# Performance work log

Hardware: AMD Instinct MI355X
Metric: run time of the kernel (lower is better)

The kernel has to match this reference:

```python
import jax, jax.numpy as jnp
import numpy as np

HEAD_DIM = 64
N_HEADS = 16
D_S = N_HEADS * HEAD_DIM  # 1024
D_Z = 128


def setup_inputs() -> dict:
    key = jax.random.key(0)
    ks = jax.random.split(key, 12)
    B, S = 1, 1024
    sc = 0.02
    return {
        "s": jax.random.normal(ks[0], (B, S, D_S), jnp.float32),
        "z": jax.random.normal(ks[1], (B, S, S, D_Z), jnp.float32),
        "wq": jax.random.normal(ks[2], (N_HEADS * HEAD_DIM, D_S), jnp.float32) * sc,
        "bq": jax.random.normal(ks[3], (N_HEADS * HEAD_DIM,), jnp.float32) * sc,
        "wk": jax.random.normal(ks[4], (N_HEADS * HEAD_DIM, D_S), jnp.float32) * sc,
        "wv": jax.random.normal(ks[5], (N_HEADS * HEAD_DIM, D_S), jnp.float32) * sc,
        "wg": jax.random.normal(ks[6], (N_HEADS * HEAD_DIM, D_S), jnp.float32) * sc,
        "z_norm_w": jnp.ones((D_Z,), jnp.float32),
        "z_norm_b": jnp.zeros((D_Z,), jnp.float32),
        "wz": jax.random.normal(ks[7], (N_HEADS, D_Z), jnp.float32) * sc,
        "wo": jax.random.normal(ks[8], (D_S, N_HEADS * HEAD_DIM), jnp.float32) * sc,
    }


def _layer_norm(x, w, b, eps=1e-5):
    mu = jnp.mean(x, axis=-1, keepdims=True)
    var = jnp.var(x, axis=-1, keepdims=True)
    return (x - mu) * jax.lax.rsqrt(var + eps) * w + b


def reference(s, z, wq, bq, wk, wv, wg, z_norm_w, z_norm_b, wz, wo):
    B, S, _ = s.shape
    H, hd = N_HEADS, HEAD_DIM
    # fused QKV projection (only q has bias in the original)
    q = (s @ wq.T + bq).reshape(B, S, H, hd)
    k = (s @ wk.T).reshape(B, S, H, hd)
    v = (s @ wv.T).reshape(B, S, H, hd)
    # pair bias: LN(z) -> linear D_Z -> H, permute to [B,H,S,S]
    zn = _layer_norm(z, z_norm_w, z_norm_b)
    bias = jnp.einsum("bijz,hz->bhij", zn, wz)  # [B,H,S,S]
    # attention with pair bias (net math: qk/sqrt(d) + bias)
    scores = jnp.einsum("bihd,bjhd->bhij", q, k) * (hd ** -0.5) + bias
    attn = jax.nn.softmax(scores, axis=-1)
    o = jnp.einsum("bhij,bjhd->bihd", attn, v).reshape(B, S, H * hd)
    # sigmoid gate then output projection
    g = jax.nn.sigmoid(s @ wg.T)
    return (o * g) @ wo.T
```

## Files before the change

### kernel.cpp

```cpp
#include <hip/hip_runtime.h>

typedef __attribute__((ext_vector_type(8))) short bf16x8;
typedef __attribute__((ext_vector_type(4))) float f32x4;

#define MFMA16(a,b,c) __builtin_amdgcn_mfma_f32_16x16x32_bf16(a,b,c,0,0,0)

__device__ __forceinline__ unsigned short f2bf(float f){
  unsigned int u = __float_as_uint(f);
  unsigned int r = (u + 0x7fffu + ((u >> 16) & 1u)) >> 16;
  return (unsigned short)r;
}
__device__ __forceinline__ float bf2f(unsigned short u){
  return __uint_as_float(((unsigned int)u) << 16);
}
__device__ __forceinline__ bf16x8 cvt8(float4 a, float4 b){
  bf16x8 t;
  t[0] = (short)f2bf(a.x); t[1] = (short)f2bf(a.y);
  t[2] = (short)f2bf(a.z); t[3] = (short)f2bf(a.w);
  t[4] = (short)f2bf(b.x); t[5] = (short)f2bf(b.y);
  t[6] = (short)f2bf(b.z); t[7] = (short)f2bf(b.w);
  return t;
}

__global__ __launch_bounds__(256) void prep_kernel(
    const float* __restrict__ s, const float* __restrict__ wq,
    const float* __restrict__ wk, const float* __restrict__ wv,
    const float* __restrict__ wg, const float* __restrict__ wo,
    const float* __restrict__ wz, const float* __restrict__ znw,
    const float* __restrict__ znb,
    unsigned short* __restrict__ sb, unsigned short* __restrict__ Wp,
    unsigned short* __restrict__ wob,
    unsigned short* __restrict__ wzp, float* __restrict__ c12)
{
  __shared__ float r1[256], r2[256];
  if (blockIdx.x == 6144) {
    int t = threadIdx.x; int h = t >> 4; int k0 = (t & 15) * 8;
    float p1 = 0.f, p2 = 0.f;
    for (int e = 0; e < 8; e++) {
      float wvv = wz[h*128 + k0 + e];
      float w = znw[k0 + e], b = znb[k0 + e];
      wzp[h*128 + k0 + e] = f2bf(wvv * w);
      p1 += wvv * w; p2 += wvv * b;
    }
    r1[t] = p1; r2[t] = p2;
    __syncthreads();
    if ((t & 15) == 0) {
      float s1 = 0.f, s2 = 0.f;
      for (int i = 0; i < 16; i++) { s1 += r1[t + i]; s2 += r2[t + i]; }
      c12[2*h] = s1; c12[2*h + 1] = s2;
    }
    return;
  }
  const size_t M1 = 1u << 20;
  size_t base = ((size_t)blockIdx.x * 256 + threadIdx.x) * 4;
  const float* src; unsigned short* dst; size_t off;
  if (base < M1) { src = s; dst = sb; off = base; }
  else if (base < 5*M1) {
    size_t r = base - M1; int wsel = (int)(r >> 20);
    const float* wsrc0 = (wsel == 0) ? wq : (wsel == 1) ? wk : (wsel == 2) ? wv : wg;
    src = wsrc0; dst = Wp + ((size_t)wsel << 20); off = r & (M1 - 1);
  } else { src = wo; dst = wob; off = base - 5*M1; }
  float4 v = *(const float4*)(src + off);
  ushort4 o4;
  o4.x = f2bf(v.x); o4.y = f2bf(v.y); o4.z = f2bf(v.z); o4.w = f2bf(v.w);
  *(ushort4*)(dst + off) = o4;
}

__global__ __launch_bounds__(512) void bias_stream(
    const float* __restrict__ z, const unsigned short* __restrict__ wzp,
    const float* __restrict__ c12, unsigned short* __restrict__ bias)
{
  __shared__ __align__(1024) char zbuf[2 * 65536];
  __shared__ __align__(16) unsigned short bounce[8][16][20];
  int tid = threadIdx.x;
  int w = tid >> 6, lane = tid & 63;
  int jl = lane & 15, g = lane >> 4;
  int half = lane >> 5, lane31 = lane & 31;

  bf16x8 af[4];
  #pragma unroll
  for (int mk = 0; mk < 4; mk++)
    af[mk] = *(const bf16x8*)(wzp + jl*128 + mk*32 + g*8);
  float c1r[4], c2r[4];
  #pragma unroll
  for (int r = 0; r < 4; r++) {
    c1r[r] = c12[2*(g*4 + r)];
    c2r[r] = c12[2*(g*4 + r) + 1];
  }
  int hp = lane & 15, gp = lane >> 4;

  const int nsteps = 32;
  int W = blockIdx.x * 8 + w;
  int u0 = W * nsteps;

  auto stage = [&](int u, int buf) {
    int i = u >> 6, j16 = u & 63;
    const char* gw = (const char*)z + (((size_t)i*1024 + j16*16) << 9);
    char* lb = zbuf + buf*65536 + w*8192;
    #pragma unroll
    for (int c = 0; c < 8; c++) {
      int row = c*2 + half;
      unsigned pin = (unsigned)(lane31*16) ^ (unsigned)((row & 7) << 4);
      __builtin_amdgcn_global_load_lds(
          (const unsigned int*)(gw + (size_t)row*512 + pin),
          (unsigned int*)(lb + c*1024), 16, 0, 0);
    }
  };

  stage(u0, 0);
  #pragma unroll 1
  for (int step = 0; step < nsteps; ++step) {
    int u = u0 + step;
    int buf = step & 1;
    if (step + 1 < nsteps) {
      stage(u + 1, buf ^ 1);
      asm volatile("s_waitcnt vmcnt(8)" ::: "memory");
    } else {
      asm volatile("s_waitcnt vmcnt(1)" ::: "memory");
    }
    __builtin_amdgcn_sched_barrier(0);

    const char* wb = zbuf + buf*65536 + w*8192;
    unsigned key = (unsigned)((jl & 7) << 4);
    float sum = 0.f, sq = 0.f;
    bf16x8 tf[4];
    #pragma unroll
    for (int mk = 0; mk < 4; mk++) {
      unsigned x = (unsigned)(mk*128 + g*32);
      float4 a = *(const float4*)(wb + jl*512 + (x ^ key));
      float4 b = *(const float4*)(wb + jl*512 + ((x + 16) ^ key));
      sum += a.x + a.y + a.z + a.w + b.x + b.y + b.z + b.w;
      sq = fmaf(a.x, a.x, fmaf(a.y, a.y, fmaf(a.z, a.z, fmaf(a.w, a.w, sq))));
      sq = fmaf(b.x, b.x, fmaf(b.y, b.y, fmaf(b.z, b.z, fmaf(b.w, b.w, sq))));
      tf[mk] = cvt8(a, b);
    }
    sum += __shfl_xor(sum, 16); sum += __shfl_xor(sum, 32);
    sq  += __shfl_xor(sq, 16);  sq  += __shfl_xor(sq, 32);
    float mu = sum * (1.f/128.f);
    float rs = rsqrtf(sq * (1.f/128.f) - mu*mu + 1e-5f);
    f32x4 D = {0.f, 0.f, 0.f, 0.f};
    #pragma unroll
    for (int mk = 0; mk < 4; mk++)
      D = MFMA16(af[mk], tf[mk], D);

    #pragma unroll
    for (int r = 0; r < 4; r++)
      bounce[w][g*4 + r][jl] = f2bf(rs*(D[r] - mu*c1r[r]) + c2r[r]);
    asm volatile("s_waitcnt lgkmcnt(0)" ::: "memory");
    __builtin_amdgcn_sched_barrier(0);
    {
      int i = u >> 6, j16 = u & 63;
      ushort4 vv = *(const ushort4*)(&bounce[w][hp][gp*4]);
      *(ushort4*)(bias + ((size_t)hp << 20) + (size_t)i*1024 + j16*16 + gp*4) = vv;
    }
    asm volatile("s_waitcnt lgkmcnt(0)" ::: "memory");
    __builtin_amdgcn_sched_barrier(0);
  }
}

template<int MODE>
__global__ __launch_bounds__(256) void gemm_bf16(
    const unsigned short* __restrict__ A, const unsigned short* __restrict__ Bm,
    int M, int N, int K,
    const float* __restrict__ bq,
    unsigned short* __restrict__ qb, unsigned short* __restrict__ kb,
    unsigned short* __restrict__ vT, unsigned short* __restrict__ gb,
    float* __restrict__ outF)
{
  int lane = threadIdx.x & 63;
  int w = threadIdx.x >> 6;
  int lr = lane & 15, lg = lane >> 4;
  int row0 = blockIdx.y * 64 + (w & 1) * 32;
  int col0 = blockIdx.x * 128 + (w >> 1) * 64;
  f32x4 acc[2][4] = {};
  for (int kk = 0; kk < K; kk += 32) {
    bf16x8 af[2], bfr[4];
    #pragma unroll
    for (int t = 0; t < 2; t++)
      af[t] = *(const bf16x8*)(A + (size_t)(row0 + t*16 + lr) * K + kk + lg*8);
    #pragma unroll
    for (int t = 0; t < 4; t++)
      bfr[t] = *(const bf16x8*)(Bm + (size_t)(col0 + t*16 + lr) * K + kk + lg*8);
    #pragma unroll
    for (int a = 0; a < 2; a++)
      #pragma unroll
      for (int b = 0; b < 4; b++)
        acc[a][b] = MFMA16(af[a], bfr[b], acc[a][b]);
  }
  #pragma unroll
  for (int a = 0; a < 2; a++)
    #pragma unroll
    for (int b = 0; b < 4; b++)
      #pragma unroll
      for (int r = 0; r < 4; r++) {
        int m = row0 + a*16 + lg*4 + r;
        int n = col0 + b*16 + lr;
        float v = acc[a][b][r];
        if (MODE == 0) {
          if (n < 1024)      { v = (v + bq[n]) * 0.125f; qb[(size_t)m*1024 + n] = f2bf(v); }
          else if (n < 2048) { kb[(size_t)m*1024 + (n-1024)] = f2bf(v); }
          else if (n < 3072) { vT[(size_t)(n-2048)*1024 + m] = f2bf(v); }
          else               { float sg = 1.f / (1.f + __expf(-v)); gb[(size_t)m*1024 + (n-3072)] = f2bf(sg); }
        } else {
          outF[(size_t)m * N + n] = v;
        }
      }
}

__global__ __launch_bounds__(256) void attn_kernel(
    const unsigned short* __restrict__ qb, const unsigned short* __restrict__ kb,
    const unsigned short* __restrict__ vT, const unsigned short* __restrict__ bias,
    float* __restrict__ op, float* __restrict__ ml, float* __restrict__ ll)
{
  __shared__ unsigned short P[4][1024];
  int lane = threadIdx.x & 63;
  int s = threadIdx.x >> 6;
  int jl = lane & 15, g = lane >> 4;
  int q0 = blockIdx.x * 16;
  int h = blockIdx.y;
  unsigned short* Pw = P[s];

  bf16x8 aq[2];
  #pragma unroll
  for (int kh = 0; kh < 2; kh++)
    aq[kh] = *(const bf16x8*)(qb + (size_t)(q0 + jl)*1024 + h*64 + kh*32 + g*8);

  f32x4 od[4] = {};
  float m = -1e30f, ss = 0.f;
  const unsigned short* bp = bias + ((size_t)h << 20);

  for (int jt = s*256; jt < s*256 + 256; jt += 64) {
    f32x4 sc[4] = {};
    #pragma unroll
    for (int jb = 0; jb < 4; jb++)
      #pragma unroll
      for (int kh = 0; kh < 2; kh++) {
        bf16x8 bk = *(const bf16x8*)(kb + (size_t)(jt + jb*16 + jl)*1024 + h*64 + kh*32 + g*8);
        sc[jb] = MFMA16(bk, aq[kh], sc[jb]);
      }
    #pragma unroll
    for (int jb = 0; jb < 4; jb++) {
      ushort4 bl = *(const ushort4*)(bp + (size_t)(q0 + jl)*1024 + jt + jb*16 + g*4);
      sc[jb][0] += bf2f(bl.x); sc[jb][1] += bf2f(bl.y);
      sc[jb][2] += bf2f(bl.z); sc[jb][3] += bf2f(bl.w);
    }

    float mx = -1e30f;
    #pragma unroll
    for (int jb = 0; jb < 4; jb++)
      #pragma unroll
      for (int r = 0; r < 4; r++) mx = fmaxf(mx, sc[jb][r]);
    mx = fmaxf(mx, __shfl_xor(mx, 16));
    mx = fmaxf(mx, __shfl_xor(mx, 32));
    float mn = fmaxf(m, mx);
    float a = __expf(m - mn);
    m = mn;
    float rsum = 0.f;
    #pragma unroll
    for (int jb = 0; jb < 4; jb++) {
      short4 pk;
      float p0 = __expf(sc[jb][0] - mn); rsum += p0; pk.x = (short)f2bf(p0);
      float p1 = __expf(sc[jb][1] - mn); rsum += p1; pk.y = (short)f2bf(p1);
      float p2 = __expf(sc[jb][2] - mn); rsum += p2; pk.z = (short)f2bf(p2);
      float p3 = __expf(sc[jb][3] - mn); rsum += p3; pk.w = (short)f2bf(p3);
      int b = jb*2 + (g >> 1);
      int bpz = b ^ (jl & 7);
      *(short4*)(Pw + jl*64 + bpz*8 + (g & 1)*4) = pk;
    }
    ss = ss * a + rsum;

    float albc[4];
    #pragma unroll
    for (int r = 0; r < 4; r++) albc[r] = __shfl(a, g*4 + r);
    #pragma unroll
    for (int db = 0; db < 4; db++)
      #pragma unroll
      for (int r = 0; r < 4; r++) od[db][r] *= albc[r];

    #pragma unroll
    for (int jh = 0; jh < 2; jh++) {
      int b = jh*4 + g;
      int bpz = b ^ (jl & 7);
      bf16x8 ap = *(const bf16x8*)(Pw + jl*64 + bpz*8);
      #pragma unroll
      for (int db = 0; db < 4; db++) {
        bf16x8 bv = *(const bf16x8*)(vT + (size_t)(h*64 + db*16 + jl)*1024 + jt + jh*32 + g*8);
        od[db] = MFMA16(ap, bv, od[db]);
      }
    }
  }

  ss += __shfl_xor(ss, 16);
  ss += __shfl_xor(ss, 32);

  size_t base = ((size_t)(s*16 + h) * 1024);
  #pragma unroll
  for (int db = 0; db < 4; db++)
    #pragma unroll
    for (int r = 0; r < 4; r++) {
      int q = q0 + g*4 + r;
      op[(base + q)*64 + db*16 + jl] = od[db][r];
    }
  if (g == 0) {
    ml[base + q0 + jl] = m;
    ll[base + q0 + jl] = ss;
  }
}

__global__ __launch_bounds__(256) void combine_kernel(
    const float* __restrict__ op, const float* __restrict__ ml,
    const float* __restrict__ ll, const unsigned short* __restrict__ gb,
    unsigned short* __restrict__ og)
{
  int t = blockIdx.x * 256 + threadIdx.x;
  int d4 = t & 15;
  int q = (t >> 4) & 1023;
  int h = t >> 14;

  float mv[4], lv[4];
  float mstar = -1e30f;
  #pragma unroll
  for (int s = 0; s < 4; s++) {
    mv[s] = ml[(size_t)(s*16 + h)*1024 + q];
    lv[s] = ll[(size_t)(s*16 + h)*1024 + q];
    mstar = fmaxf(mstar, mv[s]);
  }
  float lsum = 0.f;
  float ws[4];
  #pragma unroll
  for (int s = 0; s < 4; s++) {
    ws[s] = __expf(mv[s] - mstar);
    lsum = fmaf(ws[s], lv[s], lsum);
  }
  float inv = 1.f / lsum;

  float4 o = {0.f, 0.f, 0.f, 0.f};
  #pragma unroll
  for (int s = 0; s < 4; s++) {
    float4 p = *(const float4*)(op + ((size_t)(s*16 + h)*1024 + q)*64 + d4*4);
    o.x = fmaf(ws[s], p.x, o.x); o.y = fmaf(ws[s], p.y, o.y);
    o.z = fmaf(ws[s], p.z, o.z); o.w = fmaf(ws[s], p.w, o.w);
  }
  ushort4 gv = *(const ushort4*)(gb + (size_t)q*1024 + h*64 + d4*4);
  ushort4 r;
  r.x = f2bf(o.x * inv * bf2f(gv.x));
  r.y = f2bf(o.y * inv * bf2f(gv.y));
  r.z = f2bf(o.z * inv * bf2f(gv.z));
  r.w = f2bf(o.w * inv * bf2f(gv.w));
  *(ushort4*)(og + (size_t)q*1024 + h*64 + d4*4) = r;
}

extern "C" void kernel_launch(void* const* d_in, const int* in_sizes, int n_in,
                              void* d_out, int out_size, void* d_ws, size_t ws_size,
                              hipStream_t stream) {
  const float* s   = (const float*)d_in[0];
  const float* z   = (const float*)d_in[1];
  const float* wq  = (const float*)d_in[2];
  const float* bq  = (const float*)d_in[3];
  const float* wk  = (const float*)d_in[4];
  const float* wv  = (const float*)d_in[5];
  const float* wg  = (const float*)d_in[6];
  const float* znw = (const float*)d_in[7];
  const float* znb = (const float*)d_in[8];
  const float* wz  = (const float*)d_in[9];
  const float* wo  = (const float*)d_in[10];
  float* out = (float*)d_out;

  char* ws = (char*)d_ws;
  unsigned short* biasb = (unsigned short*)ws;
  unsigned short* qbuf  = (unsigned short*)(ws + ((size_t)64 << 20));
  unsigned short* kbuf  = (unsigned short*)(ws + ((size_t)66 << 20));
  unsigned short* vTb   = (unsigned short*)(ws + ((size_t)68 << 20));
  unsigned short* gbuf  = (unsigned short*)(ws + ((size_t)70 << 20));
  unsigned short* ogb   = (unsigned short*)(ws + ((size_t)72 << 20));
  unsigned short* sb    = (unsigned short*)(ws + ((size_t)74 << 20));
  unsigned short* Wp    = (unsigned short*)(ws + ((size_t)76 << 20));
  unsigned short* wob   = (unsigned short*)(ws + ((size_t)84 << 20));
  unsigned short* wzp   = (unsigned short*)(ws + ((size_t)86 << 20));
  float*          c12   = (float*)(ws + ((size_t)86 << 20) + 4096);
  float*          opart = (float*)(ws + ((size_t)96 << 20));
  float*          mlb   = (float*)(ws + ((size_t)112 << 20));
  float*          llb   = (float*)(ws + ((size_t)113 << 20));

  prep_kernel<<<6145, 256, 0, stream>>>(s, wq, wk, wv, wg, wo, wz, znw, znb,
                                        sb, Wp, wob, wzp, c12);
  gemm_bf16<0><<<dim3(32, 16), 256, 0, stream>>>(sb, Wp, 1024, 4096, 1024, bq,
                                                 qbuf, kbuf, vTb, gbuf, nullptr);
  bias_stream<<<256, 512, 0, stream>>>(z, wzp, c12, biasb);
  attn_kernel<<<dim3(64, 16), 256, 0, stream>>>(qbuf, kbuf, vTb, biasb, opart, mlb, llb);
  combine_kernel<<<1024, 256, 0, stream>>>(opart, mlb, llb, gbuf, ogb);
  gemm_bf16<1><<<dim3(8, 16), 256, 0, stream>>>(ogb, wob, 1024, 1024, 1024, nullptr,
                                                nullptr, nullptr, nullptr, nullptr, out);
}
```

Measured before the change: 269.5 us.

## Fuse bias stream with QKV gemm and fold combine into attention epilogue

Merges the pair-bias LayerNorm/projection streaming kernel and the QKV projection gemm into one launch with disjoint block ranges so they overlap. The bias path now loads z directly into registers with double buffering instead of async LDS staging. Attention no longer splits keys across warps; each warp handles its own 16 queries over all keys and applies normalization and the sigmoid gate in its epilogue, eliminating the partial-output buffers and combine kernel. This removes a launch and intermediate traffic, but reduces attention parallelism and may weaken the bias stream's memory latency hiding.

Result: faster. 255.3 us (-5.3%).

```diff
diff --git a/kernel.cpp b/kernel.cpp
--- a/kernel.cpp
+++ b/kernel.cpp
@@ -66,157 +66,131 @@
   *(ushort4*)(dst + off) = o4;
 }
 
-__global__ __launch_bounds__(512) void bias_stream(
+__global__ __launch_bounds__(256) void bias_gemm(
     const float* __restrict__ z, const unsigned short* __restrict__ wzp,
-    const float* __restrict__ c12, unsigned short* __restrict__ bias)
+    const float* __restrict__ c12, unsigned short* __restrict__ bias,
+    const unsigned short* __restrict__ sb, const unsigned short* __restrict__ Wp,
+    const float* __restrict__ bq,
+    unsigned short* __restrict__ qb, unsigned short* __restrict__ kb,
+    unsigned short* __restrict__ vT, unsigned short* __restrict__ gb)
 {
-  __shared__ __align__(1024) char zbuf[2 * 65536];
-  __shared__ __align__(16) unsigned short bounce[8][16][20];
+  __shared__ __align__(16) unsigned short bounce[4][16][20];
   int tid = threadIdx.x;
   int w = tid >> 6, lane = tid & 63;
   int jl = lane & 15, g = lane >> 4;
-  int half = lane >> 5, lane31 = lane & 31;
-
-  bf16x8 af[4];
-  #pragma unroll
-  for (int mk = 0; mk < 4; mk++)
-    af[mk] = *(const bf16x8*)(wzp + jl*128 + mk*32 + g*8);
-  float c1r[4], c2r[4];
-  #pragma unroll
-  for (int r = 0; r < 4; r++) {
-    c1r[r] = c12[2*(g*4 + r)];
-    c2r[r] = c12[2*(g*4 + r) + 1];
-  }
-  int hp = lane & 15, gp = lane >> 4;
-
-  const int nsteps = 32;
-  int W = blockIdx.x * 8 + w;
-  int u0 = W * nsteps;
-
-  auto stage = [&](int u, int buf) {
-    int i = u >> 6, j16 = u & 63;
-    const char* gw = (const char*)z + (((size_t)i*1024 + j16*16) << 9);
-    char* lb = zbuf + buf*65536 + w*8192;
-    #pragma unroll
-    for (int c = 0; c < 8; c++) {
-      int row = c*2 + half;
-      unsigned pin = (unsigned)(lane31*16) ^ (unsigned)((row & 7) << 4);
-      __builtin_amdgcn_global_load_lds(
-          (const unsigned int*)(gw + (size_t)row*512 + pin),
-          (unsigned int*)(lb + c*1024), 16, 0, 0);
-    }
-  };
-
-  stage(u0, 0);
-  #pragma unroll 1
-  for (int step = 0; step < nsteps; ++step) {
-    int u = u0 + step;
-    int buf = step & 1;
-    if (step + 1 < nsteps) {
-      stage(u + 1, buf ^ 1);
-      asm volatile("s_waitcnt vmcnt(8)" ::: "memory");
-    } else {
-      asm volatile("s_waitcnt vmcnt(1)" ::: "memory");
-    }
-    __builtin_amdgcn_sched_barrier(0);
-
-    const char* wb = zbuf + buf*65536 + w*8192;
-    unsigned key = (unsigned)((jl & 7) << 4);
-    float sum = 0.f, sq = 0.f;
-    bf16x8 tf[4];
-    #pragma unroll
-    for (int mk = 0; mk < 4; mk++) {
-      unsigned x = (unsigned)(mk*128 + g*32);
-      float4 a = *(const float4*)(wb + jl*512 + (x ^ key));
-      float4 b = *(const float4*)(wb + jl*512 + ((x + 16) ^ key));
-      sum += a.x + a.y + a.z + a.w + b.x + b.y + b.z + b.w;
-      sq = fmaf(a.x, a.x, fmaf(a.y, a.y, fmaf(a.z, a.z, fmaf(a.w, a.w, sq))));
-      sq = fmaf(b.x, b.x, fmaf(b.y, b.y, fmaf(b.z, b.z, fmaf(b.w, b.w, sq))));
-      tf[mk] = cvt8(a, b);
-    }
-    sum += __shfl_xor(sum, 16); sum += __shfl_xor(sum, 32);
-    sq  += __shfl_xor(sq, 16);  sq  += __shfl_xor(sq, 32);
-    float mu = sum * (1.f/128.f);
-    float rs = rsqrtf(sq * (1.f/128.f) - mu*mu + 1e-5f);
-    f32x4 D = {0.f, 0.f, 0.f, 0.f};
+
+  if (blockIdx.x < 512) {
+    bf16x8 af[4];
     #pragma unroll
     for (int mk = 0; mk < 4; mk++)
-      D = MFMA16(af[mk], tf[mk], D);
-
-    #pragma unroll
-    for (int r = 0; r < 4; r++)
-      bounce[w][g*4 + r][jl] = f2bf(rs*(D[r] - mu*c1r[r]) + c2r[r]);
-    asm volatile("s_waitcnt lgkmcnt(0)" ::: "memory");
-    __builtin_amdgcn_sched_barrier(0);
-    {
+      af[mk] = *(const bf16x8*)(wzp + jl*128 + mk*32 + g*8);
+    float c1r[4], c2r[4];
+    #pragma unroll
+    for (int r = 0; r < 4; r++) {
+      c1r[r] = c12[2*(g*4 + r)];
+      c2r[r] = c12[2*(g*4 + r) + 1];
+    }
+
+    int W = blockIdx.x * 4 + w;
+    int u0 = W * 32;
+
+    float4 A0[8], A1[8];
+
+    auto loadu = [&](int u, float4 (&A)[8]) {
       int i = u >> 6, j16 = u & 63;
-      ushort4 vv = *(const ushort4*)(&bounce[w][hp][gp*4]);
-      *(ushort4*)(bias + ((size_t)hp << 20) + (size_t)i*1024 + j16*16 + gp*4) = vv;
-    }
-    asm volatile("s_waitcnt lgkmcnt(0)" ::: "memory");
-    __builtin_amdgcn_sched_barrier(0);
-  }
-}
-
-template<int MODE>
-__global__ __launch_bounds__(256) void gemm_bf16(
-    const unsigned short* __restrict__ A, const unsigned short* __restrict__ Bm,
-    int M, int N, int K,
-    const float* __restrict__ bq,
-    unsigned short* __restrict__ qb, unsigned short* __restrict__ kb,
-    unsigned short* __restrict__ vT, unsigned short* __restrict__ gb,
-    float* __restrict__ outF)
-{
-  int lane = threadIdx.x & 63;
-  int w = threadIdx.x >> 6;
-  int lr = lane & 15, lg = lane >> 4;
-  int row0 = blockIdx.y * 64 + (w & 1) * 32;
-  int col0 = blockIdx.x * 128 + (w >> 1) * 64;
-  f32x4 acc[2][4] = {};
-  for (int kk = 0; kk < K; kk += 32) {
-    bf16x8 af[2], bfr[4];
-    #pragma unroll
-    for (int t = 0; t < 2; t++)
-      af[t] = *(const bf16x8*)(A + (size_t)(row0 + t*16 + lr) * K + kk + lg*8);
-    #pragma unroll
-    for (int t = 0; t < 4; t++)
-      bfr[t] = *(const bf16x8*)(Bm + (size_t)(col0 + t*16 + lr) * K + kk + lg*8);
+      const float* p = z + ((size_t)i*1024 + j16*16 + jl)*128 + g*8;
+      #pragma unroll
+      for (int mk = 0; mk < 4; mk++) {
+        A[2*mk]   = *(const float4*)(p + mk*32);
+        A[2*mk+1] = *(const float4*)(p + mk*32 + 4);
+      }
+    };
+    auto proc = [&](int u, float4 (&A)[8]) {
+      float sum = 0.f, sq = 0.f;
+      #pragma unroll
+      for (int t = 0; t < 8; t++) {
+        float4 v = A[t];
+        sum += v.x + v.y + v.z + v.w;
+        sq = fmaf(v.x, v.x, fmaf(v.y, v.y, fmaf(v.z, v.z, fmaf(v.w, v.w, sq))));
+      }
+      sum += __shfl_xor(sum, 16); sum += __shfl_xor(sum, 32);
+      sq  += __shfl_xor(sq, 16);  sq  += __shfl_xor(sq, 32);
+      float mu = sum * (1.f/128.f);
+      float rs = rsqrtf(sq * (1.f/128.f) - mu*mu + 1e-5f);
+      f32x4 D = {0.f, 0.f, 0.f, 0.f};
+      #pragma unroll
+      for (int mk = 0; mk < 4; mk++)
+        D = MFMA16(af[mk], cvt8(A[2*mk], A[2*mk+1]), D);
+      #pragma unroll
+      for (int r = 0; r < 4; r++)
+        bounce[w][g*4 + r][jl] = f2bf(rs*(D[r] - mu*c1r[r]) + c2r[r]);
+      asm volatile("s_waitcnt lgkmcnt(0)" ::: "memory");
+      __builtin_amdgcn_sched_barrier(0);
+      {
+        int i = u >> 6, j16 = u & 63;
+        ushort4 vv = *(const ushort4*)(&bounce[w][jl][g*4]);
+        *(ushort4*)(bias + ((size_t)jl << 20) + (size_t)i*1024 + j16*16 + g*4) = vv;
+      }
+      asm volatile("s_waitcnt lgkmcnt(0)" ::: "memory");
+      __builtin_amdgcn_sched_barrier(0);
+    };
+
+    loadu(u0, A0);
+    #pragma unroll 1
+    for (int st = 0; st < 32; st += 2) {
+      if (st + 1 < 32) loadu(u0 + st + 1, A1);
+      proc(u0 + st, A0);
+      if (st + 2 < 32) loadu(u0 + st + 2, A0);
+      proc(u0 + st + 1, A1);
+    }
+  } else {
+    int bxx = blockIdx.x - 512;
+    int bx = bxx & 31, by = bxx >> 5;
+    int lr = jl, lg = g;
+    int row0 = by * 64 + (w & 1) * 32;
+    int col0 = bx * 128 + (w >> 1) * 64;
+    f32x4 acc[2][4] = {};
+    for (int kk = 0; kk < 1024; kk += 32) {
+      bf16x8 afr[2], bfr[4];
+      #pragma unroll
+      for (int t = 0; t < 2; t++)
+        afr[t] = *(const bf16x8*)(sb + (size_t)(row0 + t*16 + lr)*1024 + kk + lg*8);
+      #pragma unroll
+      for (int t = 0; t < 4; t++)
+        bfr[t] = *(const bf16x8*)(Wp + (size_t)(col0 + t*16 + lr)*1024 + kk + lg*8);
+      #pragma unroll
+      for (int a = 0; a < 2; a++)
+        #pragma unroll
+        for (int b = 0; b < 4; b++)
+          acc[a][b] = MFMA16(afr[a], bfr[b], acc[a][b]);
+    }
     #pragma unroll
     for (int a = 0; a < 2; a++)
       #pragma unroll
       for (int b = 0; b < 4; b++)
-        acc[a][b] = MFMA16(af[a], bfr[b], acc[a][b]);
-  }
-  #pragma unroll
-  for (int a = 0; a < 2; a++)
-    #pragma unroll
-    for (int b = 0; b < 4; b++)
-      #pragma unroll
-      for (int r = 0; r < 4; r++) {
-        int m = row0 + a*16 + lg*4 + r;
-        int n = col0 + b*16 + lr;
-        float v = acc[a][b][r];
-        if (MODE == 0) {
+        #pragma unroll
+        for (int r = 0; r < 4; r++) {
+          int m = row0 + a*16 + lg*4 + r;
+          int n = col0 + b*16 + lr;
+          float v = acc[a][b][r];
           if (n < 1024)      { v = (v + bq[n]) * 0.125f; qb[(size_t)m*1024 + n] = f2bf(v); }
           else if (n < 2048) { kb[(size_t)m*1024 + (n-1024)] = f2bf(v); }
           else if (n < 3072) { vT[(size_t)(n-2048)*1024 + m] = f2bf(v); }
           else               { float sg = 1.f / (1.f + __expf(-v)); gb[(size_t)m*1024 + (n-3072)] = f2bf(sg); }
-        } else {
-          outF[(size_t)m * N + n] = v;
         }
-      }
+  }
 }
 
 __global__ __launch_bounds__(256) void attn_kernel(
     const unsigned short* __restrict__ qb, const unsigned short* __restrict__ kb,
     const unsigned short* __restrict__ vT, const unsigned short* __restrict__ bias,
-    float* __restrict__ op, float* __restrict__ ml, float* __restrict__ ll)
+    const unsigned short* __restrict__ gb, unsigned short* __restrict__ og)
 {
   __shared__ unsigned short P[4][1024];
   int lane = threadIdx.x & 63;
   int s = threadIdx.x >> 6;
   int jl = lane & 15, g = lane >> 4;
-  int q0 = blockIdx.x * 16;
+  int q0 = (blockIdx.x * 4 + s) * 16;
   int h = blockIdx.y;
   unsigned short* Pw = P[s];
 
@@ -229,7 +203,7 @@
   float m = -1e30f, ss = 0.f;
   const unsigned short* bp = bias + ((size_t)h << 20);
 
-  for (int jt = s*256; jt < s*256 + 256; jt += 64) {
+  for (int jt = 0; jt < 1024; jt += 64) {
     f32x4 sc[4] = {};
     #pragma unroll
     for (int jb = 0; jb < 4; jb++)
@@ -292,62 +266,56 @@
 
   ss += __shfl_xor(ss, 16);
   ss += __shfl_xor(ss, 32);
-
-  size_t base = ((size_t)(s*16 + h) * 1024);
+  float invb[4];
+  #pragma unroll
+  for (int r = 0; r < 4; r++)
+    invb[r] = 1.f / __shfl(ss, g*4 + r);
+
   #pragma unroll
   for (int db = 0; db < 4; db++)
     #pragma unroll
     for (int r = 0; r < 4; r++) {
       int q = q0 + g*4 + r;
-      op[(base + q)*64 + db*16 + jl] = od[db][r];
-    }
-  if (g == 0) {
-    ml[base + q0 + jl] = m;
-    ll[base + q0 + jl] = ss;
+      int d = h*64 + db*16 + jl;
+      float gv = bf2f(gb[(size_t)q*1024 + d]);
+      og[(size_t)q*1024 + d] = f2bf(od[db][r] * invb[r] * gv);
+    }
+}
+
+__global__ __launch_bounds__(256) void gemm_out(
+    const unsigned short* __restrict__ A, const unsigned short* __restrict__ Bm,
+    float* __restrict__ outF)
+{
+  int lane = threadIdx.x & 63;
+  int w = threadIdx.x >> 6;
+  int lr = lane & 15, lg = lane >> 4;
+  int row0 = blockIdx.y * 64 + (w & 1) * 32;
+  int col0 = blockIdx.x * 128 + (w >> 1) * 64;
+  f32x4 acc[2][4] = {};
+  for (int kk = 0; kk < 1024; kk += 32) {
+    bf16x8 af[2], bfr[4];
+    #pragma unroll
+    for (int t = 0; t < 2; t++)
+      af[t] = *(const bf16x8*)(A + (size_t)(row0 + t*16 + lr)*1024 + kk + lg*8);
+    #pragma unroll
+    for (int t = 0; t < 4; t++)
+      bfr[t] = *(const bf16x8*)(Bm + (size_t)(col0 + t*16 + lr)*1024 + kk + lg*8);
+    #pragma unroll
+    for (int a = 0; a < 2; a++)
+      #pragma unroll
+      for (int b = 0; b < 4; b++)
+        acc[a][b] = MFMA16(af[a], bfr[b], acc[a][b]);
   }
-}
-
-__global__ __launch_bounds__(256) void combine_kernel(
-    const float* __restrict__ op, const float* __restrict__ ml,
-    const float* __restrict__ ll, const unsigned short* __restrict__ gb,
-    unsigned short* __restrict__ og)
-{
-  int t = blockIdx.x * 256 + threadIdx.x;
-  int d4 = t & 15;
-  int q = (t >> 4) & 1023;
-  int h = t >> 14;
-
-  float mv[4], lv[4];
-  float mstar = -1e30f;
   #pragma unroll
-  for (int s = 0; s < 4; s++) {
-    mv[s] = ml[(size_t)(s*16 + h)*1024 + q];
-    lv[s] = ll[(size_t)(s*16 + h)*1024 + q];
-    mstar = fmaxf(mstar, mv[s]);
-  }
-  float lsum = 0.f;
-  float ws[4];
-  #pragma unroll
-  for (int s = 0; s < 4; s++) {
-    ws[s] = __expf(mv[s] - mstar);
-    lsum = fmaf(ws[s], lv[s], lsum);
-  }
-  float inv = 1.f / lsum;
-
-  float4 o = {0.f, 0.f, 0.f, 0.f};
-  #pragma unroll
-  for (int s = 0; s < 4; s++) {
-    float4 p = *(const float4*)(op + ((size_t)(s*16 + h)*1024 + q)*64 + d4*4);
-    o.x = fmaf(ws[s], p.x, o.x); o.y = fmaf(ws[s], p.y, o.y);
-    o.z = fmaf(ws[s], p.z, o.z); o.w = fmaf(ws[s], p.w, o.w);
-  }
-  ushort4 gv = *(const ushort4*)(gb + (size_t)q*1024 + h*64 + d4*4);
-  ushort4 r;
-  r.x = f2bf(o.x * inv * bf2f(gv.x));
-  r.y = f2bf(o.y * inv * bf2f(gv.y));
-  r.z = f2bf(o.z * inv * bf2f(gv.z));
-  r.w = f2bf(o.w * inv * bf2f(gv.w));
-  *(ushort4*)(og + (size_t)q*1024 + h*64 + d4*4) = r;
+  for (int a = 0; a < 2; a++)
+    #pragma unroll
+    for (int b = 0; b < 4; b++)
+      #pragma unroll
+      for (int r = 0; r < 4; r++) {
+        int m = row0 + a*16 + lg*4 + r;
+        int n = col0 + b*16 + lr;
+        outF[(size_t)m * 1024 + n] = acc[a][b][r];
+      }
 }
 
 extern "C" void kernel_launch(void* const* d_in, const int* in_sizes, int n_in,
@@ -378,17 +346,11 @@
   unsigned short* wob   = (unsigned short*)(ws + ((size_t)84 << 20));
   unsigned short* wzp   = (unsigned short*)(ws + ((size_t)86 << 20));
   float*          c12   = (float*)(ws + ((size_t)86 << 20) + 4096);
-  float*          opart = (float*)(ws + ((size_t)96 << 20));
-  float*          mlb   = (float*)(ws + ((size_t)112 << 20));
-  float*          llb   = (float*)(ws + ((size_t)113 << 20));
 
   prep_kernel<<<6145, 256, 0, stream>>>(s, wq, wk, wv, wg, wo, wz, znw, znb,
                                         sb, Wp, wob, wzp, c12);
-  gemm_bf16<0><<<dim3(32, 16), 256, 0, stream>>>(sb, Wp, 1024, 4096, 1024, bq,
-                                                 qbuf, kbuf, vTb, gbuf, nullptr);
-  bias_stream<<<256, 512, 0, stream>>>(z, wzp, c12, biasb);
-  attn_kernel<<<dim3(64, 16), 256, 0, stream>>>(qbuf, kbuf, vTb, biasb, opart, mlb, llb);
-  combine_kernel<<<1024, 256, 0, stream>>>(opart, mlb, llb, gbuf, ogb);
-  gemm_bf16<1><<<dim3(8, 16), 256, 0, stream>>>(ogb, wob, 1024, 1024, 1024, nullptr,
-                                                nullptr, nullptr, nullptr, nullptr, out);
-}
+  bias_gemm<<<1024, 256, 0, stream>>>(z, wzp, c12, biasb,
+                                      sb, Wp, bq, qbuf, kbuf, vTb, gbuf);
+  attn_kernel<<<dim3(16, 16), 256, 0, stream>>>(qbuf, kbuf, vTb, biasb, gbuf, ogb);
+  gemm_out<<<dim3(8, 16), 256, 0, stream>>>(ogb, wob, out);
+}
```
